# Kernel optimization log

Hardware: AMD Instinct MI355X
Metric: run time of the kernel (lower is better)

The kernel has to match this reference:

```python
import jax, jax.numpy as jnp
import numpy as np

B, G, T, C = 32, 4, 512, 256


def setup_inputs() -> dict:
    key = jax.random.key(0)
    k1, k2, k3 = jax.random.split(key, 3)
    x = jax.random.normal(k1, (B, G, T, C), dtype=jnp.float32)
    # learned per-channel params, initialized around the repo defaults 0.3 / 0.1
    w_input = 0.3 * jax.random.uniform(k2, (C,), dtype=jnp.float32) + 0.15
    w_leak = 0.1 * jax.random.uniform(k3, (C,), dtype=jnp.float32) + 0.05
    return {"x": x, "w_input": w_input, "w_leak": w_leak}


def _heaviside(v):
    # theta_forget: step function with zero gradient (matches @tf.custom_gradient)
    return jax.lax.stop_gradient((v >= 0).astype(v.dtype))


def reference(x, w_input, w_leak):
    # x: (B, G, T, C) -> flatten group into batch, scan over time
    b, g, t, c = x.shape
    V_THRESH = 1.0   # V_thresh default
    T_REF = 1.0      # t_refrectory receives self.thresh (=1) positionally
    xr = jnp.transpose(x.reshape(b * g, t, c), (1, 0, 2))  # (T, N, C)

    def step(carry, xt):
        Vm, R = carry
        R = _heaviside(Vm - V_THRESH) * T_REF + _heaviside(R - 1.0) * (R - 1.0)
        Vm = (w_input * xt + (1.0 - w_leak) * Vm) * _heaviside(-R)
        return (Vm, R), Vm

    zeros = jnp.zeros((b * g, c), dtype=x.dtype)
    _, Vs = jax.lax.scan(step, (zeros, zeros), xr)  # Vs: (T, N, C)
    return jnp.transpose(Vs, (1, 0, 2)).reshape(b, g, t, c)
```

## Files before the change

kernel.cpp:

```cpp
#include <hip/hip_runtime.h>


constexpr int T_STEPS = 512;
constexpr int CCH     = 256;
constexpr int NSEQ    = 128;
constexpr int WIN     = 16;
constexpr int NWIN    = T_STEPS / WIN;

__device__ __forceinline__ void sfence() { __builtin_amdgcn_sched_barrier(0); }

__global__ __launch_bounds__(256, 1) void lif_kernel(
    const float* __restrict__ x,
    const float* __restrict__ w_input,
    const float* __restrict__ w_leak,
    float* __restrict__ out)
{
#pragma clang fp contract(off)
    __shared__ float xw[3][WIN * CCH];

    const int tid = threadIdx.x;
    const int n   = blockIdx.x;

    const float w = w_input[tid];
    const float a = 1.0f - w_leak[tid];

    const float* xg = x   + (size_t)n * T_STEPS * CCH;
    float*       og = out + (size_t)n * T_STEPS * CCH + tid;

    auto issue = [&](int Wt) {
        float* dst0 = &xw[Wt % 3][(tid >> 6) * 256];
        const float* src0 = xg + (size_t)Wt * (WIN * CCH) + tid * 4;
#pragma unroll
        for (int i = 0; i < 4; ++i) {
            __builtin_amdgcn_global_load_lds(
                (const __attribute__((address_space(1))) void*)(src0 + i * 1024),
                (__attribute__((address_space(3))) void*)(dst0 + i * 1024),
                16, 0, 0);
        }
        sfence();
    };

    float Vm = 0.0f;

    auto compute_store = [&](int Wt) {
        const float* xb = &xw[Wt % 3][0];
        float ov[WIN];
#pragma unroll
        for (int k = 0; k < WIN; ++k) {
            const float xt = xb[k * CCH + tid];
            const float v = (w * xt) + (a * Vm);
            Vm = (Vm - 1.0f >= 0.0f) ? 0.0f : v;
            ov[k] = Vm;
        }
        sfence();
#pragma unroll
        for (int k = 0; k < WIN; ++k)
            og[(size_t)(Wt * WIN + k) * CCH] = ov[k];
        sfence();
    };

    issue(0); issue(1);
    asm volatile("s_waitcnt vmcnt(4)" ::: "memory");
    __builtin_amdgcn_s_barrier();

    issue(2);
    compute_store(0);
    asm volatile("s_waitcnt vmcnt(20)" ::: "memory");
    __builtin_amdgcn_s_barrier();

    for (int W = 1; W <= 29; ++W) {
        issue(W + 2);
        compute_store(W);
        asm volatile("s_waitcnt vmcnt(36)" ::: "memory");
        __builtin_amdgcn_s_barrier();
    }

    compute_store(30);
    asm volatile("s_waitcnt vmcnt(32)" ::: "memory");
    __builtin_amdgcn_s_barrier();

    compute_store(31);
}

extern "C" void kernel_launch(void* const* d_in, const int* in_sizes, int n_in,
                              void* d_out, int out_size, void* d_ws, size_t ws_size,
                              hipStream_t stream) {
    const float* x       = (const float*)d_in[0];
    const float* w_input = (const float*)d_in[1];
    const float* w_leak  = (const float*)d_in[2];
    float* out = (float*)d_out;

    dim3 grid(NSEQ);
    dim3 block(CCH);
    hipLaunchKernelGGL(lif_kernel, grid, block, 0, stream,
                       x, w_input, w_leak, out);
}
```

Measured before the change: 28.07 us.

## Stage outputs through LDS for 16-byte vector stores and double the window

```diff
diff --git a/kernel.cpp b/kernel.cpp
--- a/kernel.cpp
+++ b/kernel.cpp
@@ -1,10 +1,12 @@
 #include <hip/hip_runtime.h>
 
+
+typedef float f32x4 __attribute__((ext_vector_type(4)));
 
 constexpr int T_STEPS = 512;
 constexpr int CCH     = 256;
 constexpr int NSEQ    = 128;
-constexpr int WIN     = 16;
+constexpr int WIN     = 32;
 constexpr int NWIN    = T_STEPS / WIN;
 
 __device__ __forceinline__ void sfence() { __builtin_amdgcn_sched_barrier(0); }
@@ -17,21 +19,24 @@
 {
 #pragma clang fp contract(off)
     __shared__ float xw[3][WIN * CCH];
+    __shared__ float obuf[WIN * CCH];
 
     const int tid = threadIdx.x;
+    const int wv  = tid >> 6;
+    const int l   = tid & 63;
     const int n   = blockIdx.x;
 
     const float w = w_input[tid];
     const float a = 1.0f - w_leak[tid];
 
     const float* xg = x   + (size_t)n * T_STEPS * CCH;
-    float*       og = out + (size_t)n * T_STEPS * CCH + tid;
+    float*       og = out + (size_t)n * T_STEPS * CCH;
 
     auto issue = [&](int Wt) {
-        float* dst0 = &xw[Wt % 3][(tid >> 6) * 256];
+        float* dst0 = &xw[Wt % 3][wv * 256];
         const float* src0 = xg + (size_t)Wt * (WIN * CCH) + tid * 4;
 #pragma unroll
-        for (int i = 0; i < 4; ++i) {
+        for (int i = 0; i < 8; ++i) {
             __builtin_amdgcn_global_load_lds(
                 (const __attribute__((address_space(1))) void*)(src0 + i * 1024),
                 (__attribute__((address_space(3))) void*)(dst0 + i * 1024),
@@ -42,44 +47,64 @@
 
     float Vm = 0.0f;
 
-    auto compute_store = [&](int Wt) {
+    auto compute = [&](int Wt) {
         const float* xb = &xw[Wt % 3][0];
-        float ov[WIN];
 #pragma unroll
         for (int k = 0; k < WIN; ++k) {
             const float xt = xb[k * CCH + tid];
             const float v = (w * xt) + (a * Vm);
             Vm = (Vm - 1.0f >= 0.0f) ? 0.0f : v;
-            ov[k] = Vm;
+            obuf[k * CCH + tid] = Vm;
         }
         sfence();
+    };
+
+    auto stores = [&](int Wt) {
 #pragma unroll
-        for (int k = 0; k < WIN; ++k)
-            og[(size_t)(Wt * WIN + k) * CCH] = ov[k];
+        for (int i = 0; i < 8; ++i) {
+            const int r = 4 * i + wv;
+            const f32x4 vv = *(const f32x4*)&obuf[r * CCH + 4 * l];
+            *(f32x4*)(og + (size_t)(Wt * WIN + r) * CCH + 4 * l) = vv;
+        }
+        sfence();
+    };
+
+    auto lds_barrier = [&] {
+        sfence();
+        asm volatile("s_waitcnt lgkmcnt(0)" ::: "memory");
+        __builtin_amdgcn_s_barrier();
         sfence();
     };
 
     issue(0); issue(1);
-    asm volatile("s_waitcnt vmcnt(4)" ::: "memory");
+    asm volatile("s_waitcnt vmcnt(8)" ::: "memory");
     __builtin_amdgcn_s_barrier();
 
     issue(2);
-    compute_store(0);
-    asm volatile("s_waitcnt vmcnt(20)" ::: "memory");
+    compute(0);
+    lds_barrier();
+    stores(0);
+    asm volatile("s_waitcnt vmcnt(16)" ::: "memory");
     __builtin_amdgcn_s_barrier();
 
-    for (int W = 1; W <= 29; ++W) {
+    for (int W = 1; W <= NWIN - 3; ++W) {
         issue(W + 2);
-        compute_store(W);
-        asm volatile("s_waitcnt vmcnt(36)" ::: "memory");
+        compute(W);
+        lds_barrier();
+        stores(W);
+        asm volatile("s_waitcnt vmcnt(24)" ::: "memory");
         __builtin_amdgcn_s_barrier();
     }
 
-    compute_store(30);
-    asm volatile("s_waitcnt vmcnt(32)" ::: "memory");
+    compute(NWIN - 2);
+    lds_barrier();
+    stores(NWIN - 2);
+    asm volatile("s_waitcnt vmcnt(16)" ::: "memory");
     __builtin_amdgcn_s_barrier();
 
-    compute_store(31);
+    compute(NWIN - 1);
+    lds_barrier();
+    stores(NWIN - 1);
 }
 
 extern "C" void kernel_launch(void* const* d_in, const int* in_sizes, int n_in,
```

Measured after the change: 39.37 us. 1.4x slower.

## Add dedicated producer wavefront for LDS prefetch, separate from compute wavefronts

Applied to the files above, without the earlier changes.

```diff
diff --git a/kernel.cpp b/kernel.cpp
--- a/kernel.cpp
+++ b/kernel.cpp
@@ -5,81 +5,73 @@
 constexpr int CCH     = 256;
 constexpr int NSEQ    = 128;
 constexpr int WIN     = 16;
-constexpr int NWIN    = T_STEPS / WIN;
+constexpr int K       = 4;
+constexpr int NW      = T_STEPS / WIN;
 
 __device__ __forceinline__ void sfence() { __builtin_amdgcn_sched_barrier(0); }
 
-__global__ __launch_bounds__(256, 1) void lif_kernel(
+__global__ __launch_bounds__(320, 1) void lif_kernel(
     const float* __restrict__ x,
     const float* __restrict__ w_input,
     const float* __restrict__ w_leak,
     float* __restrict__ out)
 {
 #pragma clang fp contract(off)
-    __shared__ float xw[3][WIN * CCH];
+    __shared__ float xw[K][WIN * CCH];
 
-    const int tid = threadIdx.x;
-    const int n   = blockIdx.x;
+    const int tid  = threadIdx.x;
+    const int wv   = tid >> 6;
+    const int lane = tid & 63;
+    const int n    = blockIdx.x;
 
-    const float w = w_input[tid];
-    const float a = 1.0f - w_leak[tid];
+    if (wv == 4) {
+        const float* xg = x + (size_t)n * T_STEPS * CCH + lane * 4;
+        auto issue = [&](int W) {
+            const float* s0 = xg + (size_t)W * WIN * CCH;
+            float* d0 = &xw[W & 3][0];
+#pragma unroll
+            for (int i = 0; i < WIN; ++i) {
+                __builtin_amdgcn_global_load_lds(
+                    (const __attribute__((address_space(1))) void*)(s0 + i * CCH),
+                    (__attribute__((address_space(3))) void*)(d0 + i * CCH),
+                    16, 0, 0);
+            }
+            sfence();
+        };
 
-    const float* xg = x   + (size_t)n * T_STEPS * CCH;
-    float*       og = out + (size_t)n * T_STEPS * CCH + tid;
+        issue(0); issue(1); issue(2);
+        for (int W = 0; W < NW; ++W) {
+            const int rem = NW - 1 - W;
+            if (rem >= 2)      asm volatile("s_waitcnt vmcnt(32)" ::: "memory");
+            else if (rem == 1) asm volatile("s_waitcnt vmcnt(16)" ::: "memory");
+            else               asm volatile("s_waitcnt vmcnt(0)"  ::: "memory");
+            sfence();
+            __builtin_amdgcn_s_barrier();
+            sfence();
+            if (W + 3 < NW) issue(W + 3);
+        }
+    } else {
+        const int ch = wv * 64 + lane;
+        const float w = w_input[ch];
+        const float a = 1.0f - w_leak[ch];
+        float* og = out + (size_t)n * T_STEPS * CCH + ch;
+        float Vm = 0.0f;
 
-    auto issue = [&](int Wt) {
-        float* dst0 = &xw[Wt % 3][(tid >> 6) * 256];
-        const float* src0 = xg + (size_t)Wt * (WIN * CCH) + tid * 4;
+        for (int W = 0; W < NW; ++W) {
+            sfence();
+            __builtin_amdgcn_s_barrier();
+            sfence();
+            const float* xb = &xw[W & 3][0];
 #pragma unroll
-        for (int i = 0; i < 4; ++i) {
-            __builtin_amdgcn_global_load_lds(
-                (const __attribute__((address_space(1))) void*)(src0 + i * 1024),
-                (__attribute__((address_space(3))) void*)(dst0 + i * 1024),
-                16, 0, 0);
+            for (int k = 0; k < WIN; ++k) {
+                const float xt = xb[k * CCH + ch];
+                const float v = (w * xt) + (a * Vm);
+                Vm = (Vm - 1.0f >= 0.0f) ? 0.0f : v;
+                og[(size_t)(W * WIN + k) * CCH] = Vm;
+            }
+            sfence();
         }
-        sfence();
-    };
-
-    float Vm = 0.0f;
-
-    auto compute_store = [&](int Wt) {
-        const float* xb = &xw[Wt % 3][0];
-        float ov[WIN];
-#pragma unroll
-        for (int k = 0; k < WIN; ++k) {
-            const float xt = xb[k * CCH + tid];
-            const float v = (w * xt) + (a * Vm);
-            Vm = (Vm - 1.0f >= 0.0f) ? 0.0f : v;
-            ov[k] = Vm;
-        }
-        sfence();
-#pragma unroll
-        for (int k = 0; k < WIN; ++k)
-            og[(size_t)(Wt * WIN + k) * CCH] = ov[k];
-        sfence();
-    };
-
-    issue(0); issue(1);
-    asm volatile("s_waitcnt vmcnt(4)" ::: "memory");
-    __builtin_amdgcn_s_barrier();
-
-    issue(2);
-    compute_store(0);
-    asm volatile("s_waitcnt vmcnt(20)" ::: "memory");
-    __builtin_amdgcn_s_barrier();
-
-    for (int W = 1; W <= 29; ++W) {
-        issue(W + 2);
-        compute_store(W);
-        asm volatile("s_waitcnt vmcnt(36)" ::: "memory");
-        __builtin_amdgcn_s_barrier();
     }
-
-    compute_store(30);
-    asm volatile("s_waitcnt vmcnt(32)" ::: "memory");
-    __builtin_amdgcn_s_barrier();
-
-    compute_store(31);
 }
 
 extern "C" void kernel_launch(void* const* d_in, const int* in_sizes, int n_in,
@@ -91,7 +83,7 @@
     float* out = (float*)d_out;
 
     dim3 grid(NSEQ);
-    dim3 block(CCH);
+    dim3 block(320);
     hipLaunchKernelGGL(lif_kernel, grid, block, 0, stream,
                        x, w_input, w_leak, out);
 }
```

New measurement: 26.09 us. 7.0% less time.
